# Performance work log

Hardware: AMD Instinct MI355X
Metric: run time of the kernel (lower is better)

## Reference

```python
import jax, jax.numpy as jnp
import numpy as np

N = 8192
E = 262144
IN_SELF = 512
IN_AGG = 512
OUT = 256  # out_channels; hidden = 2*OUT = 512


def _glorot(key, shape, scale=0.05):
    return jax.random.normal(key, shape, dtype=jnp.float32) * scale


def setup_inputs() -> dict:
    key = jax.random.key(0)
    ks = jax.random.split(key, 16)
    x_self = jax.random.normal(ks[0], (N, IN_SELF), dtype=jnp.float32)
    x_neighbor = jax.random.normal(ks[1], (N, IN_AGG), dtype=jnp.float32)
    edge_index = jax.random.randint(ks[2], (2, E), 0, N, dtype=jnp.int64)
    H = 2 * OUT
    return {
        "x_self": x_self,
        "x_neighbor": x_neighbor,
        "edge_index": edge_index,
        # linear_in_self: IN_SELF -> 2*OUT
        "w_in_self": _glorot(ks[3], (IN_SELF, H)),
        "b_in_self": jnp.zeros((H,), jnp.float32),
        # linear_out_self: IN_SELF + 2*OUT -> OUT
        "w_out_self": _glorot(ks[4], (IN_SELF + H, OUT)),
        "b_out_self": jnp.zeros((OUT,), jnp.float32),
        # gcn1: IN_SELF -> 2*OUT
        "gw1": _glorot(ks[5], (IN_SELF, H)),
        "gb1": jnp.zeros((H,), jnp.float32),
        # gcn2: 2*OUT -> OUT
        "gw2": _glorot(ks[6], (H, OUT)),
        "gb2": jnp.zeros((OUT,), jnp.float32),
        # linear_out: IN_AGG + OUT -> OUT
        "w_out": _glorot(ks[7], (IN_AGG + OUT, OUT)),
        "b_out": jnp.zeros((OUT,), jnp.float32),
    }


def _gcn_norm(edge_index, n):
    # PyG GCNConv default: add self loops, symmetric deg^-1/2 normalization.
    loop = jnp.arange(n, dtype=edge_index.dtype)
    src = jnp.concatenate([edge_index[0], loop])
    dst = jnp.concatenate([edge_index[1], loop])
    deg = jax.ops.segment_sum(jnp.ones_like(dst, dtype=jnp.float32), dst, num_segments=n)
    dinv = jnp.where(deg > 0, jax.lax.rsqrt(deg), 0.0)
    norm = dinv[src] * dinv[dst]  # [E+N]
    return src, dst, norm


def _gcn(x, w, b, src, dst, norm, n):
    h = x @ w                                   # [N, out]
    msg = h[src] * norm[:, None]                # gather + scale
    agg = jax.ops.segment_sum(msg, dst, num_segments=n)
    return agg + b


def reference(x_self, x_neighbor, edge_index,
              w_in_self, b_in_self, w_out_self, b_out_self,
              gw1, gb1, gw2, gb2, w_out, b_out):
    n = x_self.shape[0]
    src, dst, norm = _gcn_norm(edge_index, n)
    # linear branch
    l1 = jax.nn.relu(x_self @ w_in_self + b_in_self)
    l1 = jnp.concatenate([x_self, l1], axis=1) @ w_out_self + b_out_self
    # GCN branch
    g1 = _gcn(x_self, gw1, gb1, src, dst, norm, n)
    g2 = _gcn(g1, gw2, gb2, src, dst, norm, n)
    x2 = jnp.concatenate([x_neighbor, g2], axis=1) @ w_out + b_out
    # concat latent, dense inner-product decode
    z = jnp.concatenate([l1, x2], axis=1)       # [N, 2*OUT]
    return jax.nn.sigmoid(z @ z.T)              # [N, N]
```

## Files before the change

kernel.cpp:

```cpp
#include <hip/hip_runtime.h>
#include <cstdint>
#include <cstddef>

#define NNODE 8192
#define NEDGE 262144

typedef __attribute__((ext_vector_type(8))) short bf16x8;
typedef __attribute__((ext_vector_type(4))) float f32x4;

__device__ __forceinline__ unsigned short f2bf_rn(float x) {
    unsigned u = __float_as_uint(x);
    u = (u + 0x7FFFu + ((u >> 16) & 1u)) >> 16;
    return (unsigned short)u;
}
__device__ __forceinline__ float bf2f(unsigned short h) {
    return __uint_as_float(((unsigned)h) << 16);
}

__device__ __forceinline__ void gload16(const char* gp, char* lp) {
    __builtin_amdgcn_global_load_lds((const __attribute__((address_space(1))) void*)gp,
                                     (__attribute__((address_space(3))) void*)lp, 16, 0, 0);
}


__global__ void k_count(const int* __restrict__ dst, int* __restrict__ cnt, int n) {
    int i = blockIdx.x * blockDim.x + threadIdx.x;
    if (i < n) atomicAdd(&cnt[dst[i]], 1);
}

__global__ __launch_bounds__(256) void k_scan(const int* __restrict__ cnt,
                                              int* __restrict__ row_start,
                                              int* __restrict__ cursor,
                                              float* __restrict__ dinv) {
    __shared__ int part[256];
    const int tid = threadIdx.x;
    const int PER = NNODE / 256;
    const int base = tid * PER;
    int loc[PER];
    int sum = 0;
#pragma unroll
    for (int i = 0; i < PER; ++i) { loc[i] = cnt[base + i]; sum += loc[i]; }
    part[tid] = sum;
    __syncthreads();
    if (tid == 0) {
        int r = 0;
        for (int i = 0; i < 256; ++i) { int t = part[i]; part[i] = r; r += t; }
    }
    __syncthreads();
    int run = part[tid];
#pragma unroll
    for (int i = 0; i < PER; ++i) {
        row_start[base + i] = run;
        cursor[base + i] = run;
        dinv[base + i] = rsqrtf((float)loc[i] + 1.0f);
        run += loc[i];
    }
    if (tid == 255) row_start[NNODE] = run;
}

__global__ void k_fill_csr2(const int* __restrict__ src, const int* __restrict__ dst,
                            int* __restrict__ cursor, const float* __restrict__ dinv,
                            int* __restrict__ slist, float* __restrict__ wlist, int n) {
    int e = blockIdx.x * blockDim.x + threadIdx.x;
    if (e < n) {
        int d = dst[e];
        int s = src[e];
        int pos = atomicAdd(&cursor[d], 1);
        slist[pos] = s;
        wlist[pos] = dinv[s] * dinv[d];
    }
}

__device__ __forceinline__ void split_wt_tile(const float* __restrict__ W, int K, int N,
                                              int k0, int n0,
                                              unsigned short* __restrict__ Oh,
                                              unsigned short* __restrict__ Ol,
                                              float (*t)[33]) {
    const int c = threadIdx.x & 31, r8 = threadIdx.x >> 5;
#pragma unroll
    for (int i = 0; i < 4; ++i) {
        int r = r8 + i * 8;
        t[r][c] = W[(size_t)(k0 + r) * N + n0 + c];
    }
    __syncthreads();
#pragma unroll
    for (int i = 0; i < 4; ++i) {
        int r = r8 + i * 8;
        float x = t[c][r];
        unsigned short h = f2bf_rn(x);
        Oh[(size_t)(n0 + r) * K + k0 + c] = h;
        Ol[(size_t)(n0 + r) * K + k0 + c] = f2bf_rn(x - bf2f(h));
    }
}

__global__ __launch_bounds__(256) void k_prep(
    const float* __restrict__ x_self, const float* __restrict__ x_neighbor,
    const float* __restrict__ w_in_self, const float* __restrict__ w_out_self,
    const float* __restrict__ w_out, const float* __restrict__ gw1,
    const float* __restrict__ gw2, const float* __restrict__ gb1,
    unsigned short* __restrict__ xsh, unsigned short* __restrict__ xsl,
    unsigned short* __restrict__ xnh, unsigned short* __restrict__ xnl,
    unsigned short* __restrict__ wAt_h, unsigned short* __restrict__ wAt_l,
    unsigned short* __restrict__ wost_h, unsigned short* __restrict__ wost_l,
    unsigned short* __restrict__ wot_h, unsigned short* __restrict__ wot_l,
    float* __restrict__ bc, int* __restrict__ cnt) {
    __shared__ float t[32][33];
    const int b = blockIdx.x;
    const int tid = threadIdx.x;
    if (b < 8192) {
        const float* src = (b < 4096) ? x_self : x_neighbor;
        unsigned short* oh = (b < 4096) ? xsh : xnh;
        unsigned short* ol = (b < 4096) ? xsl : xnl;
        const int i = (b & 4095) * 256 + tid;
        float4 v = ((const float4*)src)[i];
        float x[4] = {v.x, v.y, v.z, v.w};
        unsigned short h[4], l[4];
#pragma unroll
        for (int j = 0; j < 4; ++j) {
            h[j] = f2bf_rn(x[j]);
            l[j] = f2bf_rn(x[j] - bf2f(h[j]));
        }
        ((ushort4*)oh)[i] = make_ushort4(h[0], h[1], h[2], h[3]);
        ((ushort4*)ol)[i] = make_ushort4(l[0], l[1], l[2], l[3]);
    } else if (b < 8448) {
        const int b2 = b - 8192;
        split_wt_tile(w_in_self, 512, 512, (b2 & 15) * 32, (b2 >> 4) * 32, wAt_h, wAt_l, t);
    } else if (b < 8576) {
        const int b3 = b - 8448;
        const int k0 = (b3 & 15) * 32, n0 = (b3 >> 4) * 32;
        const int nloc = tid & 31, kg = tid >> 5;
        float a[4] = {0.f, 0.f, 0.f, 0.f};
        for (int c = 0; c < 512; ++c) {
            float g2v = gw2[(size_t)c * 256 + n0 + nloc];
#pragma unroll
            for (int i = 0; i < 4; ++i)
                a[i] += gw1[(size_t)(k0 + kg * 4 + i) * 512 + c] * g2v;
        }
#pragma unroll
        for (int i = 0; i < 4; ++i) {
            unsigned short hh = f2bf_rn(a[i]);
            wAt_h[(size_t)(512 + n0 + nloc) * 512 + k0 + kg * 4 + i] = hh;
            wAt_l[(size_t)(512 + n0 + nloc) * 512 + k0 + kg * 4 + i] = f2bf_rn(a[i] - bf2f(hh));
        }
    } else if (b < 8832) {
        const int b4 = b - 8576;
        split_wt_tile(w_out_self, 1024, 256, (b4 & 31) * 32, (b4 >> 5) * 32, wost_h, wost_l, t);
    } else if (b < 9024) {
        const int b5 = b - 8832;
        split_wt_tile(w_out, 768, 256, (b5 % 24) * 32, (b5 / 24) * 32, wot_h, wot_l, t);
    } else if (b == 9024) {
        float a = 0.0f;
        for (int c = 0; c < 512; ++c) a += gb1[c] * gw2[(size_t)c * 256 + tid];
        bc[tid] = a;
    } else {
        cnt[(b - 9025) * 256 + tid] = 0;
    }
}

__device__ __forceinline__ void stage_g(char* buf,
                                        const char* aH, const char* aL, size_t strA,
                                        const char* bH, const char* bL, size_t strB,
                                        int rloc, int w) {
#pragma unroll
    for (int i = 0; i < 2; ++i) {
        const size_t r = (size_t)(rloc + i * 64);
        char* lp = buf + i * 4096 + w * 1024;
        gload16(aH + r * strA, lp);
        gload16(aL + r * strA, lp + 8192);
    }
    gload16(bH + (size_t)rloc * strB, buf + 16384 + w * 1024);
    gload16(bL + (size_t)rloc * strB, buf + 20480 + w * 1024);
}

__device__ __forceinline__ void core_2x4(const char* cur, int w, int sread, int lane,
                                         f32x4 acc[2][4]) {
    bf16x8 ah[2], al[2], bh[4], bl[4];
#pragma unroll
    for (int m = 0; m < 2; ++m) {
        const int row = w * 32 + m * 16 + (lane & 15);
        ah[m] = *(const bf16x8*)(cur + row * 64 + sread);
        al[m] = *(const bf16x8*)(cur + 8192 + row * 64 + sread);
    }
#pragma unroll
    for (int n = 0; n < 4; ++n) {
        const int row = n * 16 + (lane & 15);
        bh[n] = *(const bf16x8*)(cur + 16384 + row * 64 + sread);
        bl[n] = *(const bf16x8*)(cur + 20480 + row * 64 + sread);
    }
#pragma unroll
    for (int m = 0; m < 2; ++m)
#pragma unroll
        for (int n = 0; n < 4; ++n) {
            acc[m][n] = __builtin_amdgcn_mfma_f32_16x16x32_bf16(ah[m], bh[n], acc[m][n], 0, 0, 0);
            acc[m][n] = __builtin_amdgcn_mfma_f32_16x16x32_bf16(ah[m], bl[n], acc[m][n], 0, 0, 0);
            acc[m][n] = __builtin_amdgcn_mfma_f32_16x16x32_bf16(al[m], bh[n], acc[m][n], 0, 0, 0);
        }
}

__global__ __launch_bounds__(256) void k_gemm128_A(
    const unsigned short* __restrict__ xsh, const unsigned short* __restrict__ xsl,
    const unsigned short* __restrict__ wAt_h, const unsigned short* __restrict__ wAt_l,
    const float* __restrict__ bias,
    unsigned short* __restrict__ l1h, unsigned short* __restrict__ l1l,
    unsigned short* __restrict__ hcb) {
    __shared__ __align__(16) char smem[49152];
    const int tid = threadIdx.x, lane = tid & 63, w = tid >> 6;
    const int t0 = blockIdx.x;
    const int s = (t0 & 7) * 96 + (t0 >> 3);
    const int bm = (s / 12) * 128, bn = (s % 12) * 64;
    const int rloc = w * 16 + (lane >> 2);
    const int swz_src = ((lane & 3) ^ ((lane >> 3) & 3)) * 16;
    const int sread = ((lane >> 4) ^ ((lane >> 1) & 3)) * 16;
    const char* Ah = (const char*)xsh + (size_t)bm * 1024 + swz_src;
    const char* Al = (const char*)xsl + (size_t)bm * 1024 + swz_src;
    const char* Bh = (const char*)wAt_h + (size_t)bn * 1024 + swz_src;
    const char* Bl = (const char*)wAt_l + (size_t)bn * 1024 + swz_src;

    f32x4 acc[2][4] = {};
    stage_g(smem,         Ah,      Al,      1024, Bh,      Bl,      1024, rloc, w);
    stage_g(smem + 24576, Ah + 64, Al + 64, 1024, Bh + 64, Bl + 64, 1024, rloc, w);
    for (int ks = 0; ks < 16; ++ks) {
        if (ks < 15) asm volatile("s_waitcnt vmcnt(6)" ::: "memory");
        else         asm volatile("s_waitcnt vmcnt(0)" ::: "memory");
        __builtin_amdgcn_s_barrier();
        __builtin_amdgcn_sched_barrier(0);
        core_2x4(smem + (ks & 1) * 24576, w, sread, lane, acc);
        __builtin_amdgcn_sched_barrier(0);
        __builtin_amdgcn_s_barrier();
        if (ks < 14) {
            const int kb = (ks + 2) * 64;
            stage_g(smem + (ks & 1) * 24576, Ah + kb, Al + kb, 1024,
                    Bh + kb, Bl + kb, 1024, rloc, w);
        }
    }

    const int rj = (lane >> 4) * 4, cc = lane & 15;
#pragma unroll
    for (int m = 0; m < 2; ++m) {
#pragma unroll
        for (int n = 0; n < 4; ++n) {
            const int col = bn + n * 16 + cc;
#pragma unroll
            for (int j = 0; j < 4; ++j) {
                const int row = bm + w * 32 + m * 16 + rj + j;
                float x = acc[m][n][j];
                if (col < 512) {
                    x += bias[col];
                    x = fmaxf(x, 0.0f);
                    unsigned short h = f2bf_rn(x);
                    l1h[(size_t)row * 512 + col] = h;
                    l1l[(size_t)row * 512 + col] = f2bf_rn(x - bf2f(h));
                } else {
                    hcb[(size_t)row * 256 + (col - 512)] = f2bf_rn(x);
                }
            }
        }
    }
}

__global__ __launch_bounds__(256) void k_gemm128_Z(
    const unsigned short* __restrict__ xsh, const unsigned short* __restrict__ xsl,
    const unsigned short* __restrict__ l1h, const unsigned short* __restrict__ l1l,
    const unsigned short* __restrict__ xnh, const unsigned short* __restrict__ xnl,
    const unsigned short* __restrict__ g2h, const unsigned short* __restrict__ g2l,
    const unsigned short* __restrict__ wost_h, const unsigned short* __restrict__ wost_l,
    const unsigned short* __restrict__ wot_h, const unsigned short* __restrict__ wot_l,
    const float* __restrict__ b_out_self, const float* __restrict__ b_out,
    unsigned short* __restrict__ zhi, unsigned short* __restrict__ zlo) {
    __shared__ __align__(16) char smem[49152];
    const int t0 = blockIdx.x;
    const int s = (t0 & 7) * 64 + (t0 >> 3);
    const int half = s & 1;
    const int rem = s >> 1;
    const int bn = (rem & 3) * 64;
    const int bm = (rem >> 2) * 128;
    const int tid = threadIdx.x, lane = tid & 63, w = tid >> 6;
    const int rloc = w * 16 + (lane >> 2);
    const int swz_src = ((lane & 3) ^ ((lane >> 3) & 3)) * 16;
    const int sread = ((lane >> 4) ^ ((lane >> 1) & 3)) * 16;

    const unsigned short *A1h, *A1l, *A2h, *A2l, *Wh, *Wl;
    const float* bias;
    int Ktot;
    size_t strA2, strB;
    if (half == 0) {
        A1h = xsh; A1l = xsl; A2h = l1h; A2l = l1l; strA2 = 1024;
        Wh = wost_h; Wl = wost_l; strB = 2048; Ktot = 1024; bias = b_out_self;
    } else {
        A1h = xnh; A1l = xnl; A2h = g2h; A2l = g2l; strA2 = 512;
        Wh = wot_h; Wl = wot_l; strB = 1536; Ktot = 768; bias = b_out;
    }
    const int nsteps = Ktot / 32;
    const char* Bh = (const char*)Wh + (size_t)bn * strB + swz_src;
    const char* Bl = (const char*)Wl + (size_t)bn * strB + swz_src;

    auto asrc = [&](int k0, const char*& sh, const char*& sl, size_t& st) {
        if (k0 < 512) {
            sh = (const char*)A1h + (size_t)bm * 1024 + (size_t)k0 * 2 + swz_src;
            sl = (const char*)A1l + (size_t)bm * 1024 + (size_t)k0 * 2 + swz_src;
            st = 1024;
        } else {
            sh = (const char*)A2h + (size_t)bm * strA2 + (size_t)(k0 - 512) * 2 + swz_src;
            sl = (const char*)A2l + (size_t)bm * strA2 + (size_t)(k0 - 512) * 2 + swz_src;
            st = strA2;
        }
    };

    f32x4 acc[2][4] = {};
    {
        const char *sh, *sl; size_t st;
        asrc(0, sh, sl, st);
        stage_g(smem, sh, sl, st, Bh, Bl, strB, rloc, w);
        asrc(32, sh, sl, st);
        stage_g(smem + 24576, sh, sl, st, Bh + 64, Bl + 64, strB, rloc, w);
    }
    for (int ks = 0; ks < nsteps; ++ks) {
        if (ks < nsteps - 1) asm volatile("s_waitcnt vmcnt(6)" ::: "memory");
        else                 asm volatile("s_waitcnt vmcnt(0)" ::: "memory");
        __builtin_amdgcn_s_barrier();
        __builtin_amdgcn_sched_barrier(0);
        core_2x4(smem + (ks & 1) * 24576, w, sread, lane, acc);
        __builtin_amdgcn_sched_barrier(0);
        __builtin_amdgcn_s_barrier();
        if (ks + 2 < nsteps) {
            const char *sh, *sl; size_t st;
            asrc((ks + 2) * 32, sh, sl, st);
            stage_g(smem + (ks & 1) * 24576, sh, sl, st,
                    Bh + (size_t)(ks + 2) * 64, Bl + (size_t)(ks + 2) * 64, strB, rloc, w);
        }
    }

    const int rj = (lane >> 4) * 4, cc = lane & 15;
    const int zoff = half * 256;
#pragma unroll
    for (int m = 0; m < 2; ++m) {
#pragma unroll
        for (int n = 0; n < 4; ++n) {
            const int col = bn + n * 16 + cc;
            const float bv = bias[col];
#pragma unroll
            for (int j = 0; j < 4; ++j) {
                const int row = bm + w * 32 + m * 16 + rj + j;
                float x = acc[m][n][j] + bv;
                unsigned short h = f2bf_rn(x);
                zhi[(size_t)row * 512 + zoff + col] = h;
                zlo[(size_t)row * 512 + zoff + col] = f2bf_rn(x - bf2f(h));
            }
        }
    }
}

template <int MODE>
__global__ __launch_bounds__(256) void k_agg4(
    const int* __restrict__ row_start, const int* __restrict__ slist,
    const float* __restrict__ wlist, const float* __restrict__ dinv,
    const unsigned short* __restrict__ h,
    const float* __restrict__ bc, const float* __restrict__ b2,
    unsigned short* __restrict__ t1,
    unsigned short* __restrict__ oh, unsigned short* __restrict__ ol) {
    const int n = blockIdx.x * 4 + (threadIdx.x >> 6);
    const int lane = threadIdx.x & 63;
    const int c0 = lane * 4;
    const float di = dinv[n];

    ushort4 selfv = ((const ushort4*)(h + (size_t)n * 256))[lane];
    float acc[4];
    acc[0] = di * di * bf2f(selfv.x);
    acc[1] = di * di * bf2f(selfv.y);
    acc[2] = di * di * bf2f(selfv.z);
    acc[3] = di * di * bf2f(selfv.w);
    float sv = di * di;

    const int e0 = row_start[n], e1 = row_start[n + 1];
    int j = e0;
    for (; j + 4 <= e1; j += 4) {
        int ss[4];
        float ww[4];
        ushort4 rv[4];
#pragma unroll
        for (int u = 0; u < 4; ++u) { ss[u] = slist[j + u]; ww[u] = wlist[j + u]; }
#pragma unroll
        for (int u = 0; u < 4; ++u)
            rv[u] = ((const ushort4*)(h + (size_t)ss[u] * 256))[lane];
#pragma unroll
        for (int u = 0; u < 4; ++u) {
            acc[0] += ww[u] * bf2f(rv[u].x);
            acc[1] += ww[u] * bf2f(rv[u].y);
            acc[2] += ww[u] * bf2f(rv[u].z);
            acc[3] += ww[u] * bf2f(rv[u].w);
            if (MODE) sv += ww[u];
        }
    }
    for (; j < e1; ++j) {
        const float wv = wlist[j];
        ushort4 rv = ((const ushort4*)(h + (size_t)slist[j] * 256))[lane];
        acc[0] += wv * bf2f(rv.x);
        acc[1] += wv * bf2f(rv.y);
        acc[2] += wv * bf2f(rv.z);
        acc[3] += wv * bf2f(rv.w);
        if (MODE) sv += wv;
    }

    if (MODE == 0) {
        ushort4 o;
        o.x = f2bf_rn(acc[0]); o.y = f2bf_rn(acc[1]);
        o.z = f2bf_rn(acc[2]); o.w = f2bf_rn(acc[3]);
        ((ushort4*)(t1 + (size_t)n * 256))[lane] = o;
    } else {
        ushort4 vh, vl;
        float x0 = acc[0] + sv * bc[c0 + 0] + b2[c0 + 0];
        float x1 = acc[1] + sv * bc[c0 + 1] + b2[c0 + 1];
        float x2 = acc[2] + sv * bc[c0 + 2] + b2[c0 + 2];
        float x3 = acc[3] + sv * bc[c0 + 3] + b2[c0 + 3];
        vh.x = f2bf_rn(x0); vl.x = f2bf_rn(x0 - bf2f(vh.x));
        vh.y = f2bf_rn(x1); vl.y = f2bf_rn(x1 - bf2f(vh.y));
        vh.z = f2bf_rn(x2); vl.z = f2bf_rn(x2 - bf2f(vh.z));
        vh.w = f2bf_rn(x3); vl.w = f2bf_rn(x3 - bf2f(vh.w));
        ((ushort4*)(oh + (size_t)n * 256))[lane] = vh;
        ((ushort4*)(ol + (size_t)n * 256))[lane] = vl;
    }
}

__device__ __forceinline__ void zzt_stage(char* buf, const char* s0, const char* s1,
                                          const char* s2, const char* s3,
                                          int rloc, int swz_src, int w, int kbyte) {
    const char* srcs[4] = {s0, s1, s2, s3};
#pragma unroll
    for (int tile = 0; tile < 4; ++tile) {
#pragma unroll
        for (int i = 0; i < 2; ++i) {
            const char* gp = srcs[tile] + (size_t)(rloc + i * 64) * 1024 + kbyte + swz_src;
            char* lp = buf + tile * 8192 + i * 4096 + w * 1024;
            gload16(gp, lp);
        }
    }
}

__global__ __launch_bounds__(256) void k_zzt_mfma(const unsigned short* __restrict__ zhi,
                                                  const unsigned short* __restrict__ zlo,
                                                  float* __restrict__ out) {
    __shared__ __align__(16) char smem[65536];
    const int tid = threadIdx.x;
    const int lane = tid & 63;
    const int w = tid >> 6;
    const int wr = w >> 1, wc = w & 1;

    const int t0 = blockIdx.x;
    const int t = (t0 & 7) * 260 + (t0 >> 3);
    int bi = (int)((sqrtf(8.0f * (float)t + 1.0f) - 1.0f) * 0.5f);
    while ((bi + 1) * (bi + 2) / 2 <= t) ++bi;
    while (bi * (bi + 1) / 2 > t) --bi;
    const int bj = t - bi * (bi + 1) / 2;

    const char* s0 = (const char*)zhi + (size_t)(bi * 128) * 1024;
    const char* s1 = (const char*)zlo + (size_t)(bi * 128) * 1024;
    const char* s2 = (const char*)zhi + (size_t)(bj * 128) * 1024;
    const char* s3 = (const char*)zlo + (size_t)(bj * 128) * 1024;

    const int rloc = w * 16 + (lane >> 2);
    const int swz_src = ((lane & 3) ^ ((lane >> 3) & 3)) * 16;
    const int sread = ((lane >> 4) ^ ((lane >> 1) & 3)) * 16;

    f32x4 acc[4][4] = {};

    zzt_stage(smem,         s0, s1, s2, s3, rloc, swz_src, w, 0);
    zzt_stage(smem + 32768, s0, s1, s2, s3, rloc, swz_src, w, 64);

    for (int ks = 0; ks < 16; ++ks) {
        if (ks < 15) asm volatile("s_waitcnt vmcnt(8)" ::: "memory");
        else         asm volatile("s_waitcnt vmcnt(0)" ::: "memory");
        __builtin_amdgcn_s_barrier();
        __builtin_amdgcn_sched_barrier(0);
        const char* cur = smem + (ks & 1) * 32768;

        bf16x8 ah[4], al[4], bh[4], bl[4];
        const char* pa = cur + (wr * 64 + (lane & 15)) * 64 + sread;
        const char* pb = cur + 16384 + (wc * 64 + (lane & 15)) * 64 + sread;
#pragma unroll
        for (int m = 0; m < 4; ++m) {
            ah[m] = *(const bf16x8*)(pa + m * 1024);
            al[m] = *(const bf16x8*)(pa + 8192 + m * 1024);
        }
#pragma unroll
        for (int n = 0; n < 4; ++n) {
            bh[n] = *(const bf16x8*)(pb + n * 1024);
            bl[n] = *(const bf16x8*)(pb + 8192 + n * 1024);
        }
        __builtin_amdgcn_s_setprio(1);
#pragma unroll
        for (int m = 0; m < 4; ++m)
#pragma unroll
            for (int n = 0; n < 4; ++n) {
                acc[m][n] = __builtin_amdgcn_mfma_f32_16x16x32_bf16(ah[m], bh[n], acc[m][n], 0, 0, 0);
                acc[m][n] = __builtin_amdgcn_mfma_f32_16x16x32_bf16(ah[m], bl[n], acc[m][n], 0, 0, 0);
                acc[m][n] = __builtin_amdgcn_mfma_f32_16x16x32_bf16(al[m], bh[n], acc[m][n], 0, 0, 0);
            }
        __builtin_amdgcn_s_setprio(0);
        __builtin_amdgcn_sched_barrier(0);
        __builtin_amdgcn_s_barrier();
        if (ks < 14)
            zzt_stage(smem + (ks & 1) * 32768, s0, s1, s2, s3, rloc, swz_src, w,
                      (ks + 2) * 64);
    }

    const int rj = (lane >> 4) * 4;
    const int cc = lane & 15;
#pragma unroll
    for (int m = 0; m < 4; ++m) {
#pragma unroll
        for (int n = 0; n < 4; ++n) {
            float s[4];
#pragma unroll
            for (int j = 0; j < 4; ++j)
                s[j] = 1.0f / (1.0f + __expf(-acc[m][n][j]));
            const int gr0 = bi * 128 + wr * 64 + m * 16 + rj;
            const int gc  = bj * 128 + wc * 64 + n * 16 + cc;
#pragma unroll
            for (int j = 0; j < 4; ++j)
                __builtin_nontemporal_store(s[j], out + (size_t)(gr0 + j) * NNODE + gc);
            if (bi != bj) {
                const int mr = bj * 128 + wc * 64 + n * 16 + cc;
                const int mc = bi * 128 + wr * 64 + m * 16 + rj;
                f32x4 v = {s[0], s[1], s[2], s[3]};
                __builtin_nontemporal_store(v, (f32x4*)(out + (size_t)mr * NNODE + mc));
            }
        }
    }
}

extern "C" void kernel_launch(void* const* d_in, const int* in_sizes, int n_in,
                              void* d_out, int out_size, void* d_ws, size_t ws_size,
                              hipStream_t stream) {
    const float* x_self     = (const float*)d_in[0];
    const float* x_neighbor = (const float*)d_in[1];
    const int*   ei         = (const int*)d_in[2];
    const float* w_in_self  = (const float*)d_in[3];
    const float* b_in_self  = (const float*)d_in[4];
    const float* w_out_self = (const float*)d_in[5];
    const float* b_out_self = (const float*)d_in[6];
    const float* gw1        = (const float*)d_in[7];
    const float* gb1        = (const float*)d_in[8];
    const float* gw2        = (const float*)d_in[9];
    const float* gb2        = (const float*)d_in[10];
    const float* w_out      = (const float*)d_in[11];
    const float* b_out      = (const float*)d_in[12];
    float* out = (float*)d_out;

    char* ws = (char*)d_ws;
    const size_t MB = 1024 * 1024;
    const size_t KB = 1024;
    int*   cnt       = (int*)(ws + 0);
    int*   row_start = (int*)(ws + 32 * KB);
    int*   cursor    = (int*)(ws + 96 * KB);
    float* dinv      = (float*)(ws + 128 * KB);
    float* bc        = (float*)(ws + 192 * KB);
    int*   slist     = (int*)(ws + 2 * MB);
    float* wlist     = (float*)(ws + 3 * MB);
    unsigned short* xsh = (unsigned short*)(ws + 4 * MB);
    unsigned short* xsl = (unsigned short*)(ws + 12 * MB);
    unsigned short* xnh = (unsigned short*)(ws + 20 * MB);
    unsigned short* xnl = (unsigned short*)(ws + 28 * MB);
    unsigned short* l1h = (unsigned short*)(ws + 36 * MB);
    unsigned short* l1l = (unsigned short*)(ws + 44 * MB);
    unsigned short* hcb = (unsigned short*)(ws + 52 * MB);
    unsigned short* t1b = (unsigned short*)(ws + 60 * MB);
    unsigned short* g2h = (unsigned short*)(ws + 68 * MB);
    unsigned short* g2l = (unsigned short*)(ws + 72 * MB);
    unsigned short* zhi = (unsigned short*)(ws + 76 * MB);
    unsigned short* zlo = (unsigned short*)(ws + 84 * MB);
    unsigned short* wAt_h = (unsigned short*)(ws + 92 * MB);
    unsigned short* wAt_l = (unsigned short*)(ws + 93 * MB);
    unsigned short* wost_h = (unsigned short*)(ws + 94 * MB);
    unsigned short* wost_l = (unsigned short*)(ws + 95 * MB);
    unsigned short* wot_h  = (unsigned short*)(ws + 96 * MB);
    unsigned short* wot_l  = (unsigned short*)(ws + 97 * MB);

    const int* srcA = ei;
    const int* dstA = ei + NEDGE;

    k_prep<<<9057, 256, 0, stream>>>(x_self, x_neighbor, w_in_self, w_out_self, w_out,
                                     gw1, gw2, gb1, xsh, xsl, xnh, xnl,
                                     wAt_h, wAt_l, wost_h, wost_l, wot_h, wot_l, bc, cnt);

    k_count<<<NEDGE / 256, 256, 0, stream>>>(dstA, cnt, NEDGE);
    k_scan<<<1, 256, 0, stream>>>(cnt, row_start, cursor, dinv);
    k_fill_csr2<<<NEDGE / 256, 256, 0, stream>>>(srcA, dstA, cursor, dinv, slist, wlist, NEDGE);

    k_gemm128_A<<<768, 256, 0, stream>>>(
        xsh, xsl, wAt_h, wAt_l, b_in_self, l1h, l1l, hcb);

    k_agg4<0><<<NNODE / 4, 256, 0, stream>>>(row_start, slist, wlist, dinv, hcb,
                                             nullptr, nullptr, t1b, nullptr, nullptr);
    k_agg4<1><<<NNODE / 4, 256, 0, stream>>>(row_start, slist, wlist, dinv, t1b,
                                             bc, gb2, nullptr, g2h, g2l);

    k_gemm128_Z<<<512, 256, 0, stream>>>(
        xsh, xsl, l1h, l1l, xnh, xnl, g2h, g2l,
        wost_h, wost_l, wot_h, wot_l, b_out_self, b_out, zhi, zlo);

    k_zzt_mfma<<<2080, 256, 0, stream>>>(zhi, zlo, out);
}
```

Before: 354.2 us.

## Replace split-bf16 Z·Zᵀ decode with two-level int8 quantized MFMA

Z is now stored in fp32, and a new kernel quantizes each row to int8 with a per-row scale plus an int8 residual scaled by 256. The Z·Zᵀ kernel then uses i8 MFMA (16x16x64) with three products per tile, and rescales and applies the sigmoid in the epilogue. This halves the operand bytes and doubles K per instruction compared with split bf16, so there are half as many K steps. The costs are an extra kernel, an fp32 Z round trip through memory, and lower accuracy (roughly 15 bits effective) that may reduce tolerance margin.

```diff
diff --git a/kernel.cpp b/kernel.cpp
--- a/kernel.cpp
+++ b/kernel.cpp
@@ -7,6 +7,7 @@
 
 typedef __attribute__((ext_vector_type(8))) short bf16x8;
 typedef __attribute__((ext_vector_type(4))) float f32x4;
+typedef __attribute__((ext_vector_type(4))) int i32x4;
 
 __device__ __forceinline__ unsigned short f2bf_rn(float x) {
     unsigned u = __float_as_uint(x);
@@ -266,7 +267,7 @@
     const unsigned short* __restrict__ wost_h, const unsigned short* __restrict__ wost_l,
     const unsigned short* __restrict__ wot_h, const unsigned short* __restrict__ wot_l,
     const float* __restrict__ b_out_self, const float* __restrict__ b_out,
-    unsigned short* __restrict__ zhi, unsigned short* __restrict__ zlo) {
+    float* __restrict__ zf) {
     __shared__ __align__(16) char smem[49152];
     const int t0 = blockIdx.x;
     const int s = (t0 & 7) * 64 + (t0 >> 3);
@@ -341,10 +342,7 @@
 #pragma unroll
             for (int j = 0; j < 4; ++j) {
                 const int row = bm + w * 32 + m * 16 + rj + j;
-                float x = acc[m][n][j] + bv;
-                unsigned short h = f2bf_rn(x);
-                zhi[(size_t)row * 512 + zoff + col] = h;
-                zlo[(size_t)row * 512 + zoff + col] = f2bf_rn(x - bf2f(h));
+                zf[(size_t)row * 512 + zoff + col] = acc[m][n][j] + bv;
             }
         }
     }
@@ -421,24 +419,60 @@
     }
 }
 
-__device__ __forceinline__ void zzt_stage(char* buf, const char* s0, const char* s1,
-                                          const char* s2, const char* s3,
-                                          int rloc, int swz_src, int w, int kbyte) {
+__global__ __launch_bounds__(256) void k_quant(const float* __restrict__ z,
+                                               signed char* __restrict__ qa,
+                                               signed char* __restrict__ qb,
+                                               float* __restrict__ scl) {
+    const int n = blockIdx.x * 4 + (threadIdx.x >> 6);
+    const int lane = threadIdx.x & 63;
+    const float* zr = z + (size_t)n * 512;
+    float4 v0 = ((const float4*)zr)[lane * 2];
+    float4 v1 = ((const float4*)zr)[lane * 2 + 1];
+    float xs[8] = {v0.x, v0.y, v0.z, v0.w, v1.x, v1.y, v1.z, v1.w};
+    float m = 0.0f;
+#pragma unroll
+    for (int j = 0; j < 8; ++j) m = fmaxf(m, fabsf(xs[j]));
+#pragma unroll
+    for (int off = 32; off; off >>= 1) m = fmaxf(m, __shfl_xor(m, off));
+    m = fmaxf(m, 1e-20f);
+    const float s = m * (1.0f / 127.0f);
+    const float inv = 127.0f / m;
+    if (lane == 0) scl[n] = s;
+    unsigned long long pa = 0, pb = 0;
+#pragma unroll
+    for (int j = 0; j < 8; ++j) {
+        float af = rintf(xs[j] * inv);
+        af = fminf(fmaxf(af, -127.0f), 127.0f);
+        int ia = (int)af;
+        float r = xs[j] - af * s;
+        int ib = (int)rintf(r * inv * 256.0f);
+        ib = ib > 127 ? 127 : (ib < -128 ? -128 : ib);
+        pa |= ((unsigned long long)(unsigned char)(ia & 0xff)) << (8 * j);
+        pb |= ((unsigned long long)(unsigned char)(ib & 0xff)) << (8 * j);
+    }
+    *(unsigned long long*)(qa + (size_t)n * 512 + lane * 8) = pa;
+    *(unsigned long long*)(qb + (size_t)n * 512 + lane * 8) = pb;
+}
+
+__device__ __forceinline__ void q8_stage(char* buf, const char* s0, const char* s1,
+                                         const char* s2, const char* s3,
+                                         int rloc, int swz_src, int w, int kbyte) {
     const char* srcs[4] = {s0, s1, s2, s3};
 #pragma unroll
     for (int tile = 0; tile < 4; ++tile) {
 #pragma unroll
         for (int i = 0; i < 2; ++i) {
-            const char* gp = srcs[tile] + (size_t)(rloc + i * 64) * 1024 + kbyte + swz_src;
+            const char* gp = srcs[tile] + (size_t)(rloc + i * 64) * 512 + kbyte + swz_src;
             char* lp = buf + tile * 8192 + i * 4096 + w * 1024;
             gload16(gp, lp);
         }
     }
 }
 
-__global__ __launch_bounds__(256) void k_zzt_mfma(const unsigned short* __restrict__ zhi,
-                                                  const unsigned short* __restrict__ zlo,
-                                                  float* __restrict__ out) {
+__global__ __launch_bounds__(256) void k_zzt_q8(const signed char* __restrict__ qa,
+                                                const signed char* __restrict__ qb,
+                                                const float* __restrict__ scl,
+                                                float* __restrict__ out) {
     __shared__ __align__(16) char smem[65536];
     const int tid = threadIdx.x;
     const int lane = tid & 63;
@@ -452,67 +486,75 @@
     while (bi * (bi + 1) / 2 > t) --bi;
     const int bj = t - bi * (bi + 1) / 2;
 
-    const char* s0 = (const char*)zhi + (size_t)(bi * 128) * 1024;
-    const char* s1 = (const char*)zlo + (size_t)(bi * 128) * 1024;
-    const char* s2 = (const char*)zhi + (size_t)(bj * 128) * 1024;
-    const char* s3 = (const char*)zlo + (size_t)(bj * 128) * 1024;
+    const char* s0 = (const char*)qa + (size_t)(bi * 128) * 512;
+    const char* s1 = (const char*)qb + (size_t)(bi * 128) * 512;
+    const char* s2 = (const char*)qa + (size_t)(bj * 128) * 512;
+    const char* s3 = (const char*)qb + (size_t)(bj * 128) * 512;
 
     const int rloc = w * 16 + (lane >> 2);
     const int swz_src = ((lane & 3) ^ ((lane >> 3) & 3)) * 16;
     const int sread = ((lane >> 4) ^ ((lane >> 1) & 3)) * 16;
 
-    f32x4 acc[4][4] = {};
-
-    zzt_stage(smem,         s0, s1, s2, s3, rloc, swz_src, w, 0);
-    zzt_stage(smem + 32768, s0, s1, s2, s3, rloc, swz_src, w, 64);
-
-    for (int ks = 0; ks < 16; ++ks) {
-        if (ks < 15) asm volatile("s_waitcnt vmcnt(8)" ::: "memory");
-        else         asm volatile("s_waitcnt vmcnt(0)" ::: "memory");
+    i32x4 acc0[4][4] = {};
+    i32x4 acc1[4][4] = {};
+
+    q8_stage(smem,         s0, s1, s2, s3, rloc, swz_src, w, 0);
+    q8_stage(smem + 32768, s0, s1, s2, s3, rloc, swz_src, w, 64);
+
+    for (int ks = 0; ks < 8; ++ks) {
+        if (ks < 7) asm volatile("s_waitcnt vmcnt(8)" ::: "memory");
+        else        asm volatile("s_waitcnt vmcnt(0)" ::: "memory");
         __builtin_amdgcn_s_barrier();
         __builtin_amdgcn_sched_barrier(0);
         const char* cur = smem + (ks & 1) * 32768;
 
-        bf16x8 ah[4], al[4], bh[4], bl[4];
+        i32x4 ai[4], av[4], aj[4], bv[4];
         const char* pa = cur + (wr * 64 + (lane & 15)) * 64 + sread;
         const char* pb = cur + 16384 + (wc * 64 + (lane & 15)) * 64 + sread;
 #pragma unroll
         for (int m = 0; m < 4; ++m) {
-            ah[m] = *(const bf16x8*)(pa + m * 1024);
-            al[m] = *(const bf16x8*)(pa + 8192 + m * 1024);
+            ai[m] = *(const i32x4*)(pa + m * 1024);
+            av[m] = *(const i32x4*)(pa + 8192 + m * 1024);
         }
 #pragma unroll
         for (int n = 0; n < 4; ++n) {
-            bh[n] = *(const bf16x8*)(pb + n * 1024);
-            bl[n] = *(const bf16x8*)(pb + 8192 + n * 1024);
+            aj[n] = *(const i32x4*)(pb + n * 1024);
+            bv[n] = *(const i32x4*)(pb + 8192 + n * 1024);
         }
         __builtin_amdgcn_s_setprio(1);
 #pragma unroll
         for (int m = 0; m < 4; ++m)
 #pragma unroll
             for (int n = 0; n < 4; ++n) {
-                acc[m][n] = __builtin_amdgcn_mfma_f32_16x16x32_bf16(ah[m], bh[n], acc[m][n], 0, 0, 0);
-                acc[m][n] = __builtin_amdgcn_mfma_f32_16x16x32_bf16(ah[m], bl[n], acc[m][n], 0, 0, 0);
-                acc[m][n] = __builtin_amdgcn_mfma_f32_16x16x32_bf16(al[m], bh[n], acc[m][n], 0, 0, 0);
+                acc0[m][n] = __builtin_amdgcn_mfma_i32_16x16x64_i8(ai[m], aj[n], acc0[m][n], 0, 0, 0);
+                acc1[m][n] = __builtin_amdgcn_mfma_i32_16x16x64_i8(ai[m], bv[n], acc1[m][n], 0, 0, 0);
+                acc1[m][n] = __builtin_amdgcn_mfma_i32_16x16x64_i8(av[m], aj[n], acc1[m][n], 0, 0, 0);
             }
         __builtin_amdgcn_s_setprio(0);
         __builtin_amdgcn_sched_barrier(0);
         __builtin_amdgcn_s_barrier();
-        if (ks < 14)
-            zzt_stage(smem + (ks & 1) * 32768, s0, s1, s2, s3, rloc, swz_src, w,
-                      (ks + 2) * 64);
+        if (ks < 6)
+            q8_stage(smem + (ks & 1) * 32768, s0, s1, s2, s3, rloc, swz_src, w,
+                     (ks + 2) * 64);
     }
 
     const int rj = (lane >> 4) * 4;
     const int cc = lane & 15;
+    float sJ[4];
+#pragma unroll
+    for (int n = 0; n < 4; ++n) sJ[n] = scl[bj * 128 + wc * 64 + n * 16 + cc];
 #pragma unroll
     for (int m = 0; m < 4; ++m) {
 #pragma unroll
         for (int n = 0; n < 4; ++n) {
             float s[4];
 #pragma unroll
-            for (int j = 0; j < 4; ++j)
-                s[j] = 1.0f / (1.0f + __expf(-acc[m][n][j]));
+            for (int j = 0; j < 4; ++j) {
+                const float sI = scl[bi * 128 + wr * 64 + m * 16 + rj + j];
+                const float sc = sI * sJ[n] *
+                    ((float)acc0[m][n][j] + (float)acc1[m][n][j] * 0.00390625f);
+                s[j] = 1.0f / (1.0f + __expf(-sc));
+            }
             const int gr0 = bi * 128 + wr * 64 + m * 16 + rj;
             const int gc  = bj * 128 + wc * 64 + n * 16 + cc;
 #pragma unroll
@@ -566,14 +608,16 @@
     unsigned short* t1b = (unsigned short*)(ws + 60 * MB);
     unsigned short* g2h = (unsigned short*)(ws + 68 * MB);
     unsigned short* g2l = (unsigned short*)(ws + 72 * MB);
-    unsigned short* zhi = (unsigned short*)(ws + 76 * MB);
-    unsigned short* zlo = (unsigned short*)(ws + 84 * MB);
+    float*          zf  = (float*)(ws + 76 * MB);
     unsigned short* wAt_h = (unsigned short*)(ws + 92 * MB);
     unsigned short* wAt_l = (unsigned short*)(ws + 93 * MB);
     unsigned short* wost_h = (unsigned short*)(ws + 94 * MB);
     unsigned short* wost_l = (unsigned short*)(ws + 95 * MB);
     unsigned short* wot_h  = (unsigned short*)(ws + 96 * MB);
     unsigned short* wot_l  = (unsigned short*)(ws + 97 * MB);
+    signed char* qa  = (signed char*)(ws + 100 * MB);
+    signed char* qb  = (signed char*)(ws + 104 * MB);
+    float*       scl = (float*)(ws + 108 * MB);
 
     const int* srcA = ei;
     const int* dstA = ei + NEDGE;
@@ -596,7 +640,9 @@
 
     k_gemm128_Z<<<512, 256, 0, stream>>>(
         xsh, xsl, l1h, l1l, xnh, xnl, g2h, g2l,
-        wost_h, wost_l, wot_h, wot_l, b_out_self, b_out, zhi, zlo);
-
-    k_zzt_mfma<<<2080, 256, 0, stream>>>(zhi, zlo, out);
-}
+        wost_h, wost_l, wot_h, wot_l, b_out_self, b_out, zf);
+
+    k_quant<<<NNODE / 4, 256, 0, stream>>>(zf, qa, qb, scl);
+
+    k_zzt_q8<<<2080, 256, 0, stream>>>(qa, qb, scl, out);
+}
```

After: 321.7 us, median of 2. 9.2% less time.
